# Kernel tuning notes

Measured on AMD Instinct MI355X. Metric: run time of the kernel, lower is better.

## Reference

```python
import jax, jax.numpy as jnp
import numpy as np
from jax.ops import segment_sum

N = 100000   # nodes
E = 6400000  # edges
D = 128      # input/output feature dim (d)
H = 15       # hidden width hard-coded in the module


def setup_inputs() -> dict:
    key = jax.random.key(0)
    ks = jax.random.split(key, 10)
    x = jax.random.normal(ks[0], (N, D), dtype=jnp.float32)
    edge_index = jax.random.randint(ks[1], (2, E), 0, N, dtype=jnp.int64)
    def glorot(k, shape):
        lim = np.sqrt(6.0 / (shape[0] + shape[1]))
        return jax.random.uniform(k, shape, jnp.float32, -lim, lim)
    W1 = glorot(ks[2], (D, H)); b1 = jnp.zeros((H,), jnp.float32)
    W2 = glorot(ks[3], (H, H)); b2 = jnp.zeros((H,), jnp.float32)
    W3 = glorot(ks[4], (H, H)); b3 = jnp.zeros((H,), jnp.float32)
    Wc = glorot(ks[5], (H, D)); bc = jnp.zeros((D,), jnp.float32)
    return {"x": x, "edge_index": edge_index,
            "W1": W1, "b1": b1, "W2": W2, "b2": b2,
            "W3": W3, "b3": b3, "Wc": Wc, "bc": bc}


def _gcn_norm(edge_index, n_nodes):
    # PyG GCNConv default: add self-loops, symmetric normalization.
    loops = jnp.arange(n_nodes, dtype=edge_index.dtype)
    row = jnp.concatenate([edge_index[0], loops])  # source
    col = jnp.concatenate([edge_index[1], loops])  # target (aggregation index)
    deg = segment_sum(jnp.ones_like(col, dtype=jnp.float32), col, num_segments=n_nodes)
    dinv = jnp.where(deg > 0, jax.lax.rsqrt(deg), 0.0)
    norm = dinv[row] * dinv[col]  # [E+N]
    return row, col, norm


def _gcn_conv(x, W, b, row, col, norm, n_nodes):
    h = x @ W                                   # [N, out]
    msg = h[row] * norm[:, None]                # gather + scale
    agg = segment_sum(msg, col, num_segments=n_nodes)
    return agg + b


def reference(x, edge_index, W1, b1, W2, b2, W3, b3, Wc, bc):
    row, col, norm = _gcn_norm(edge_index, N)
    h = jax.nn.relu(_gcn_conv(x, W1, b1, row, col, norm, N))
    h = jax.nn.relu(_gcn_conv(h, W2, b2, row, col, norm, N))
    h = jax.nn.relu(_gcn_conv(h, W3, b3, row, col, norm, N))
    return h @ Wc + bc
```

## Files before the change

### kernel.cpp

```cpp
#include <hip/hip_runtime.h>
#include <hip/hip_fp16.h>

#define DD 128
#define HH 15
#define BSHIFT 8
#define BUCK (1 << BSHIFT)
#define NBUCK 391
#define CAP 18432
#define CHUNK 4096
#define ABLK 512


__global__ __launch_bounds__(512) void init_gcur(int* __restrict__ gcur) {
    int i = threadIdx.x;
    if (i < NBUCK) gcur[i] = i * CAP;
}


__global__ __launch_bounds__(512) void partA(const int* __restrict__ row, const int* __restrict__ col,
                      int* __restrict__ gcur, unsigned* __restrict__ tmp, int E) {
    __shared__ int histo[NBUCK];
    __shared__ int hbase[NBUCK];
    __shared__ int hscan[NBUCK];
    __shared__ int wsum[8];
    __shared__ int s_total;
    __shared__ unsigned staged[CHUNK];
    __shared__ int saddr[CHUNK];
    int tid = threadIdx.x;
    int start = blockIdx.x * CHUNK;
    for (int i = tid; i < NBUCK; i += ABLK) histo[i] = 0;
    __syncthreads();
    unsigned pk[8]; unsigned short lp[8]; unsigned short bk[8];
    for (int k = 0; k < 8; ++k) {
        int e = start + k * ABLK + tid;
        bk[k] = 0xFFFF;
        if (e < E) {
            int cc = col[e];
            int b = cc >> BSHIFT;
            int rr = row[e];
            pk[k] = (unsigned)rr | ((unsigned)(cc & (BUCK - 1)) << 17);
            bk[k] = (unsigned short)b;
            lp[k] = (unsigned short)atomicAdd(&histo[b], 1);
        }
    }
    __syncthreads();
    int lane = tid & 63, wv = tid >> 6;
    int v = (tid < NBUCK) ? histo[tid] : 0;
    int s = v;
#pragma unroll
    for (int off = 1; off < 64; off <<= 1) {
        int u = __shfl_up(s, off, 64);
        if (lane >= off) s += u;
    }
    if (lane == 63) wsum[wv] = s;
    __syncthreads();
    if (tid == 0) {
        int r = 0;
        for (int i = 0; i < 8; ++i) { int u = wsum[i]; wsum[i] = r; r += u; }
        s_total = r;
    }
    __syncthreads();
    if (tid < NBUCK) {
        int excl = s + wsum[wv] - v;
        hscan[tid] = excl;
        if (v > 0) hbase[tid] = atomicAdd(&gcur[tid], v);
    }
    __syncthreads();
    for (int k = 0; k < 8; ++k) {
        if (bk[k] != 0xFFFF) {
            int b = bk[k];
            int slot = hscan[b] + lp[k];
            saddr[slot]  = min(hbase[b] + lp[k], NBUCK * CAP - 1);
            staged[slot] = pk[k];
        }
    }
    __syncthreads();
    int tot = s_total;
    for (int k = tid; k < tot; k += ABLK)
        tmp[saddr[k]] = staged[k];
}


__global__ __launch_bounds__(512) void scanC(const int* __restrict__ gcur,
                                             int* __restrict__ cbase,
                                             int* __restrict__ rowptr, int N) {
    __shared__ int wsum[8];
    int t = threadIdx.x, lane = t & 63, wv = t >> 6;
    int v = 0;
    if (t < NBUCK) v = min(gcur[t] - t * CAP, CAP);
    int s = v;
#pragma unroll
    for (int off = 1; off < 64; off <<= 1) {
        int u = __shfl_up(s, off, 64);
        if (lane >= off) s += u;
    }
    if (lane == 63) wsum[wv] = s;
    __syncthreads();
    int total = 0;
    if (t == 0) { int r = 0; for (int i = 0; i < 8; ++i) { int u = wsum[i]; wsum[i] = r; r += u; } total = r; }
    __syncthreads();
    if (t < NBUCK) cbase[t] = s + wsum[wv] - v;
    if (t == 0) { cbase[NBUCK] = total; rowptr[N] = total; }
}


__global__ __launch_bounds__(1024) void partB(const int* __restrict__ cbase, const unsigned* __restrict__ tmp,
                      int* __restrict__ rowptr, float* __restrict__ dinv,
                      int* __restrict__ csr_row, int N) {
    __shared__ int hist[BUCK];
    __shared__ int cur[BUCK];
    __shared__ int wsum[4];
    int b = blockIdx.x;
    int node0 = b << BSHIFT;
    int nn = min(BUCK, N - node0);
    int tid = threadIdx.x;
    if (tid < BUCK) hist[tid] = 0;
    __syncthreads();
    int base = cbase[b];
    int cnt  = cbase[b + 1] - base;
    const unsigned* te = tmp + (size_t)b * CAP;
    for (int e = tid; e < cnt; e += 1024)
        atomicAdd(&hist[te[e] >> 17], 1);
    __syncthreads();
    int lane = tid & 63, wv = tid >> 6;
    int d0 = (tid < BUCK) ? hist[tid] : 0;
    int s = d0;
#pragma unroll
    for (int off = 1; off < 64; off <<= 1) {
        int u = __shfl_up(s, off, 64);
        if (lane >= off) s += u;
    }
    if (tid < BUCK && lane == 63) wsum[wv] = s;
    __syncthreads();
    if (tid == 0) { int r = 0; for (int i = 0; i < 4; ++i) { int u = wsum[i]; wsum[i] = r; r += u; } }
    __syncthreads();
    if (tid < BUCK) {
        int excl = s + wsum[wv] - d0;
        cur[tid] = base + excl;
        if (tid < nn) {
            rowptr[node0 + tid] = base + excl;
            dinv[node0 + tid] = rsqrtf((float)(d0 + 1));
        }
    }
    __syncthreads();
    for (int e = tid; e < cnt; e += 1024) {
        unsigned v2 = te[e];
        int lc = (int)(v2 >> 17);
        int pos = atomicAdd(&cur[lc], 1);
        csr_row[pos] = (int)(v2 & 0x1FFFFu);
    }
}


__global__ void gemm1_kernel(const float* __restrict__ x, const float* __restrict__ W,
                             const float* __restrict__ dinv, __half* __restrict__ hs) {
    __shared__ float Wl[DD * HH];
    __shared__ float xs[16 * DD];
    int tid = threadIdx.x;
    for (int i = tid; i < DD * HH; i += 256) Wl[i] = W[i];
    size_t base = (size_t)blockIdx.x * 16 * DD;
    const float4* xv = (const float4*)(x + base);
    float4* xsv = (float4*)xs;
    xsv[tid]       = xv[tid];
    xsv[tid + 256] = xv[tid + 256];
    __syncthreads();
    int g = tid >> 4, f = tid & 15;
    int n = blockIdx.x * 16 + g;
    float val = 0.f;
    if (f < HH) {
        const float* xrow = xs + g * DD;
        float acc = 0.f;
#pragma unroll 8
        for (int k = 0; k < DD; ++k) acc += xrow[k] * Wl[k * HH + f];
        val = acc * dinv[n];
    }
    hs[(size_t)n * 16 + f] = __float2half(val);
}


__device__ inline void accU(float4& a0, float4& a1, const uint4& u) {
    float2 f0 = __half22float2(*(const __half2*)&u.x);
    float2 f1 = __half22float2(*(const __half2*)&u.y);
    float2 f2 = __half22float2(*(const __half2*)&u.z);
    float2 f3 = __half22float2(*(const __half2*)&u.w);
    a0.x += f0.x; a0.y += f0.y; a0.z += f1.x; a0.w += f1.y;
    a1.x += f2.x; a1.y += f2.y; a1.z += f3.x; a1.w += f3.y;
}

__device__ inline float4 shfl_down4(float4 v, int off) {
    v.x = __shfl_down(v.x, off, 64);
    v.y = __shfl_down(v.y, off, 64);
    v.z = __shfl_down(v.z, off, 64);
    v.w = __shfl_down(v.w, off, 64);
    return v;
}

template <int FUSE>
__global__ __launch_bounds__(256, 2)
void aggregate_kernel(const int* __restrict__ rowptr, const int* __restrict__ csr_row,
                      const float* __restrict__ dinv, const __half* __restrict__ hs,
                      const float* __restrict__ bias, const float* __restrict__ W,
                      const float* __restrict__ bc,
                      __half* __restrict__ hsout, float* __restrict__ outF, int N) {
    __shared__ float Wl[FUSE == 2 ? HH * DD : 256];
    __shared__ float bs[16];
    __shared__ float bcs[FUSE == 2 ? DD : 1];
    __shared__ float sout[FUSE == 2 ? 16 * DD : 1];
    int tid = threadIdx.x;
    if (FUSE == 1) {
        int k = tid >> 4, f = tid & 15;
        Wl[tid] = (k < HH && f < HH) ? W[k * HH + f] : 0.f;
        if (tid < 16) bs[tid] = (tid < HH) ? bias[tid] : 0.f;
        __syncthreads();
    } else if (FUSE == 2) {
        for (int i = tid; i < HH * DD; i += 256) Wl[i] = W[i];
        if (tid < 16) bs[tid] = (tid < HH) ? bias[tid] : 0.f;
        if (tid < DD) bcs[tid] = bc[tid];
        __syncthreads();
    }
    int wid = (blockIdx.x * 256 + tid) >> 6;
    int lane = tid & 63;
    int sub = lane & 15;
    int c = wid * 4 + (lane >> 4);
    int q = sub & 1, eg = sub >> 1;
    int s = 0, epe = 0;
    if (c < N) { s = rowptr[c]; epe = rowptr[c + 1]; }
    const uint4* h8 = (const uint4*)hs;
    float4 a0 = make_float4(0.f, 0.f, 0.f, 0.f), a1 = a0;
    int e = s + eg;
    for (; e + 56 < epe; e += 64) {
        int i0 = csr_row[e];      int i1 = csr_row[e + 8];
        int i2 = csr_row[e + 16]; int i3 = csr_row[e + 24];
        int i4 = csr_row[e + 32]; int i5 = csr_row[e + 40];
        int i6 = csr_row[e + 48]; int i7 = csr_row[e + 56];
        uint4 v0 = h8[((size_t)i0 << 1) + q];
        uint4 v1 = h8[((size_t)i1 << 1) + q];
        uint4 v2 = h8[((size_t)i2 << 1) + q];
        uint4 v3 = h8[((size_t)i3 << 1) + q];
        uint4 v4 = h8[((size_t)i4 << 1) + q];
        uint4 v5 = h8[((size_t)i5 << 1) + q];
        uint4 v6 = h8[((size_t)i6 << 1) + q];
        uint4 v7 = h8[((size_t)i7 << 1) + q];
        accU(a0, a1, v0); accU(a0, a1, v1); accU(a0, a1, v2); accU(a0, a1, v3);
        accU(a0, a1, v4); accU(a0, a1, v5); accU(a0, a1, v6); accU(a0, a1, v7);
    }
    for (; e + 8 < epe; e += 16) {
        int i0 = csr_row[e]; int i1 = csr_row[e + 8];
        uint4 v0 = h8[((size_t)i0 << 1) + q];
        uint4 v1 = h8[((size_t)i1 << 1) + q];
        accU(a0, a1, v0); accU(a0, a1, v1);
    }
    if (e < epe) {
        uint4 v0 = h8[((size_t)csr_row[e] << 1) + q];
        accU(a0, a1, v0);
    }
#define RED4(off) { float4 t0_ = shfl_down4(a0, off); float4 t1_ = shfl_down4(a1, off); \
                    a0.x += t0_.x; a0.y += t0_.y; a0.z += t0_.z; a0.w += t0_.w; \
                    a1.x += t1_.x; a1.y += t1_.y; a1.z += t1_.z; a1.w += t1_.w; }
    RED4(8) RED4(4) RED4(2)
#undef RED4
    float d = (c < N) ? dinv[c] : 0.f;
    float4 o0 = make_float4(0.f, 0.f, 0.f, 0.f), o1 = o0;
    if (sub < 2 && c < N) {
        uint4 su = h8[((size_t)c << 1) + q];
        float2 s0 = __half22float2(*(const __half2*)&su.x);
        float2 s1 = __half22float2(*(const __half2*)&su.y);
        float2 s2 = __half22float2(*(const __half2*)&su.z);
        float2 s3 = __half22float2(*(const __half2*)&su.w);
        o0.x = d * (a0.x + s0.x); o0.y = d * (a0.y + s0.y);
        o0.z = d * (a0.z + s1.x); o0.w = d * (a0.w + s1.y);
        o1.x = d * (a1.x + s2.x); o1.y = d * (a1.y + s2.y);
        o1.z = d * (a1.z + s3.x); o1.w = d * (a1.w + s3.y);
        int bb = q * 8;
        o0.x = fmaxf(o0.x + bs[bb + 0], 0.f); o0.y = fmaxf(o0.y + bs[bb + 1], 0.f);
        o0.z = fmaxf(o0.z + bs[bb + 2], 0.f); o0.w = fmaxf(o0.w + bs[bb + 3], 0.f);
        o1.x = fmaxf(o1.x + bs[bb + 4], 0.f); o1.y = fmaxf(o1.y + bs[bb + 5], 0.f);
        o1.z = fmaxf(o1.z + bs[bb + 6], 0.f); o1.w = fmaxf(o1.w + bs[bb + 7], 0.f);
    }
    int base = lane & ~15;
    float va[8], vb[8];
    va[0] = __shfl(o0.x, base, 64); va[1] = __shfl(o0.y, base, 64);
    va[2] = __shfl(o0.z, base, 64); va[3] = __shfl(o0.w, base, 64);
    va[4] = __shfl(o1.x, base, 64); va[5] = __shfl(o1.y, base, 64);
    va[6] = __shfl(o1.z, base, 64); va[7] = __shfl(o1.w, base, 64);
    vb[0] = __shfl(o0.x, base + 1, 64); vb[1] = __shfl(o0.y, base + 1, 64);
    vb[2] = __shfl(o0.z, base + 1, 64); vb[3] = __shfl(o0.w, base + 1, 64);
    vb[4] = __shfl(o1.x, base + 1, 64); vb[5] = __shfl(o1.y, base + 1, 64);
    vb[6] = __shfl(o1.z, base + 1, 64); vb[7] = __shfl(o1.w, base + 1, 64);
    if (FUSE == 1) {
        float acc = 0.f;
#pragma unroll
        for (int k = 0; k < 8; ++k) acc += va[k] * Wl[k * 16 + sub];
#pragma unroll
        for (int k = 0; k < 8; ++k) acc += vb[k] * Wl[(8 + k) * 16 + sub];
        if (c < N) hsout[(size_t)c * 16 + sub] = __float2half(acc * d);
    } else if (FUSE == 2) {
        int nl = (tid >> 4);
#pragma unroll
        for (int j = 0; j < 8; ++j) {
            int f = sub + 16 * j;
            float acc = bcs[f];
#pragma unroll
            for (int k = 0; k < 8; ++k)  acc += va[k] * Wl[k * DD + f];
#pragma unroll
            for (int k = 0; k < 7; ++k)  acc += vb[k] * Wl[(8 + k) * DD + f];
            sout[nl * DD + f] = acc;
        }
        __syncthreads();
        int n0 = blockIdx.x * 16;
        const float4* sv = (const float4*)sout;
#pragma unroll
        for (int r = 0; r < 2; ++r) {
            int idx = tid + 256 * r;
            int node = idx >> 5, rem = idx & 31;
            if (n0 + node < N)
                ((float4*)outF)[((size_t)(n0 + node) * DD >> 2) + rem] = sv[idx];
        }
    }
}


extern "C" void kernel_launch(void* const* d_in, const int* in_sizes, int n_in,
                              void* d_out, int out_size, void* d_ws, size_t ws_size,
                              hipStream_t stream) {
    const float* x  = (const float*)d_in[0];
    const int*   ei = (const int*)d_in[1];
    const float* W1 = (const float*)d_in[2];
    const float* b1 = (const float*)d_in[3];
    const float* W2 = (const float*)d_in[4];
    const float* b2 = (const float*)d_in[5];
    const float* W3 = (const float*)d_in[6];
    const float* b3 = (const float*)d_in[7];
    const float* Wc = (const float*)d_in[8];
    const float* bc = (const float*)d_in[9];
    float* out = (float*)d_out;

    int N = in_sizes[0] / DD;
    int E = in_sizes[1] / 2;
    const int* row = ei;
    const int* col = ei + E;

    char* ws = (char*)d_ws;
    size_t off = 0;
    auto alloc = [&](size_t bytes) {
        void* p = ws + off;
        off += (bytes + 255) & ~(size_t)255;
        return p;
    };
    float*    dinv    = (float*)   alloc((size_t)N * 4);
    int*      rowptr  = (int*)     alloc((size_t)(N + 1) * 4);
    int*      gcur    = (int*)     alloc((size_t)NBUCK * 4);
    int*      cbase   = (int*)     alloc((size_t)(NBUCK + 1) * 4);
    int*      csr_row = (int*)     alloc((size_t)E * 4 + 256);
    unsigned* tmp     = (unsigned*)alloc((size_t)NBUCK * CAP * 4);
    (void)n_in; (void)out_size; (void)ws_size;

    __half* hsA = (__half*)tmp;
    __half* hsB = (__half*)((char*)tmp + (size_t)N * 32);

    int eblocks = (E + CHUNK - 1) / CHUNK;

    init_gcur<<<1, 512, 0, stream>>>(gcur);
    partA<<<eblocks, ABLK, 0, stream>>>(row, col, gcur, tmp, E);
    scanC<<<1, 512, 0, stream>>>(gcur, cbase, rowptr, N);
    partB<<<NBUCK, 1024, 0, stream>>>(cbase, tmp, rowptr, dinv, csr_row, N);

    int nb16 = (N + 15) / 16;
    int aggblocks = (N + 15) / 16;

    gemm1_kernel<<<nb16, 256, 0, stream>>>(x, W1, dinv, hsA);
    aggregate_kernel<1><<<aggblocks, 256, 0, stream>>>(rowptr, csr_row, dinv, hsA,
                                                       b1, W2, nullptr, hsB, nullptr, N);
    aggregate_kernel<1><<<aggblocks, 256, 0, stream>>>(rowptr, csr_row, dinv, hsB,
                                                       b2, W3, nullptr, hsA, nullptr, N);
    aggregate_kernel<2><<<aggblocks, 256, 0, stream>>>(rowptr, csr_row, dinv, hsA,
                                                       b3, Wc, bc, nullptr, out, N);
}
```

Measured before the change: 395.8 us.

## Drop global scan with bucket-local CSR, fuse first GEMM into partB, prefetch indices

The global scanC kernel is removed. Each bucket keeps its fixed CAP-strided region in csr_row, and the rows are addressed through separate rowstart/rowend arrays instead of a compact rowptr. When the workspace has room, the first-layer x@W1 projection scaled by dinv is fused into partB, which removes a launch and lets h live in dedicated buffers. The aggregation loop also software-prefetches the next batch of 8 neighbour indices. In exchange the workspace grows, partB uses more shared memory and does more work per block, and the aggregation kernel uses more registers.

```diff
diff --git a/kernel.cpp b/kernel.cpp
--- a/kernel.cpp
+++ b/kernel.cpp
@@ -9,6 +9,7 @@
 #define CAP 18432
 #define CHUNK 4096
 #define ABLK 512
+#define XSTR 132
 
 
 __global__ __launch_bounds__(512) void init_gcur(int* __restrict__ gcur) {
@@ -81,44 +82,28 @@
 }
 
 
-__global__ __launch_bounds__(512) void scanC(const int* __restrict__ gcur,
-                                             int* __restrict__ cbase,
-                                             int* __restrict__ rowptr, int N) {
-    __shared__ int wsum[8];
-    int t = threadIdx.x, lane = t & 63, wv = t >> 6;
-    int v = 0;
-    if (t < NBUCK) v = min(gcur[t] - t * CAP, CAP);
-    int s = v;
-#pragma unroll
-    for (int off = 1; off < 64; off <<= 1) {
-        int u = __shfl_up(s, off, 64);
-        if (lane >= off) s += u;
-    }
-    if (lane == 63) wsum[wv] = s;
-    __syncthreads();
-    int total = 0;
-    if (t == 0) { int r = 0; for (int i = 0; i < 8; ++i) { int u = wsum[i]; wsum[i] = r; r += u; } total = r; }
-    __syncthreads();
-    if (t < NBUCK) cbase[t] = s + wsum[wv] - v;
-    if (t == 0) { cbase[NBUCK] = total; rowptr[N] = total; }
-}
-
-
-__global__ __launch_bounds__(1024) void partB(const int* __restrict__ cbase, const unsigned* __restrict__ tmp,
-                      int* __restrict__ rowptr, float* __restrict__ dinv,
-                      int* __restrict__ csr_row, int N) {
+template <int FG>
+__global__ __launch_bounds__(1024) void partB(const int* __restrict__ gcur, const unsigned* __restrict__ tmp,
+                      int* __restrict__ rowstart, int* __restrict__ rowend,
+                      float* __restrict__ dinv, int* __restrict__ csr_row,
+                      const float* __restrict__ x, const float* __restrict__ W1,
+                      __half* __restrict__ hs, int N) {
     __shared__ int hist[BUCK];
     __shared__ int cur[BUCK];
     __shared__ int wsum[4];
+    __shared__ float sdv[BUCK];
+    __shared__ float Wl[FG ? DD * HH : 1];
+    __shared__ float xs[FG ? 64 * XSTR : 1];
     int b = blockIdx.x;
     int node0 = b << BSHIFT;
     int nn = min(BUCK, N - node0);
     int tid = threadIdx.x;
     if (tid < BUCK) hist[tid] = 0;
-    __syncthreads();
-    int base = cbase[b];
-    int cnt  = cbase[b + 1] - base;
-    const unsigned* te = tmp + (size_t)b * CAP;
+    if (FG) for (int i = tid; i < DD * HH; i += 1024) Wl[i] = W1[i];
+    __syncthreads();
+    int base = b * CAP;
+    int cnt  = min(gcur[b] - base, CAP);
+    const unsigned* te = tmp + (size_t)base;
     for (int e = tid; e < cnt; e += 1024)
         atomicAdd(&hist[te[e] >> 17], 1);
     __syncthreads();
@@ -138,8 +123,11 @@
         int excl = s + wsum[wv] - d0;
         cur[tid] = base + excl;
         if (tid < nn) {
-            rowptr[node0 + tid] = base + excl;
-            dinv[node0 + tid] = rsqrtf((float)(d0 + 1));
+            rowstart[node0 + tid] = base + excl;
+            rowend[node0 + tid]   = base + excl + d0;
+            float dv = rsqrtf((float)(d0 + 1));
+            dinv[node0 + tid] = dv;
+            sdv[tid] = dv;
         }
     }
     __syncthreads();
@@ -149,18 +137,41 @@
         int pos = atomicAdd(&cur[lc], 1);
         csr_row[pos] = (int)(v2 & 0x1FFFFu);
     }
+    if (FG) {
+        for (int p = 0; p < 4; ++p) {
+            __syncthreads();
+            for (int j = tid; j < 64 * 32; j += 1024) {
+                int r = j >> 5, cidx = j & 31;
+                int n = node0 + p * 64 + r;
+                float4 vx = make_float4(0.f, 0.f, 0.f, 0.f);
+                if (n < N) vx = ((const float4*)x)[(size_t)n * 32 + cidx];
+                ((float4*)(xs + r * XSTR))[cidx] = vx;
+            }
+            __syncthreads();
+            int r = tid >> 4, f = tid & 15;
+            int n = node0 + p * 64 + r;
+            float acc = 0.f;
+            if (f < HH) {
+                const float* xr = xs + r * XSTR;
+#pragma unroll 8
+                for (int k = 0; k < DD; ++k) acc += xr[k] * Wl[k * HH + f];
+                acc *= sdv[p * 64 + r];
+            }
+            if (n < N) hs[(size_t)n * 16 + f] = __float2half(acc);
+        }
+    }
 }
 
 
 __global__ void gemm1_kernel(const float* __restrict__ x, const float* __restrict__ W,
                              const float* __restrict__ dinv, __half* __restrict__ hs) {
     __shared__ float Wl[DD * HH];
-    __shared__ float xs[16 * DD];
+    __shared__ float xsl[16 * DD];
     int tid = threadIdx.x;
     for (int i = tid; i < DD * HH; i += 256) Wl[i] = W[i];
     size_t base = (size_t)blockIdx.x * 16 * DD;
     const float4* xv = (const float4*)(x + base);
-    float4* xsv = (float4*)xs;
+    float4* xsv = (float4*)xsl;
     xsv[tid]       = xv[tid];
     xsv[tid + 256] = xv[tid + 256];
     __syncthreads();
@@ -168,7 +179,7 @@
     int n = blockIdx.x * 16 + g;
     float val = 0.f;
     if (f < HH) {
-        const float* xrow = xs + g * DD;
+        const float* xrow = xsl + g * DD;
         float acc = 0.f;
 #pragma unroll 8
         for (int k = 0; k < DD; ++k) acc += xrow[k] * Wl[k * HH + f];
@@ -197,7 +208,8 @@
 
 template <int FUSE>
 __global__ __launch_bounds__(256, 2)
-void aggregate_kernel(const int* __restrict__ rowptr, const int* __restrict__ csr_row,
+void aggregate_kernel(const int* __restrict__ rowstart, const int* __restrict__ rowend,
+                      const int* __restrict__ csr_row,
                       const float* __restrict__ dinv, const __half* __restrict__ hs,
                       const float* __restrict__ bias, const float* __restrict__ W,
                       const float* __restrict__ bc,
@@ -224,15 +236,28 @@
     int c = wid * 4 + (lane >> 4);
     int q = sub & 1, eg = sub >> 1;
     int s = 0, epe = 0;
-    if (c < N) { s = rowptr[c]; epe = rowptr[c + 1]; }
+    if (c < N) { s = rowstart[c]; epe = rowend[c]; }
     const uint4* h8 = (const uint4*)hs;
     float4 a0 = make_float4(0.f, 0.f, 0.f, 0.f), a1 = a0;
     int e = s + eg;
-    for (; e + 56 < epe; e += 64) {
-        int i0 = csr_row[e];      int i1 = csr_row[e + 8];
-        int i2 = csr_row[e + 16]; int i3 = csr_row[e + 24];
-        int i4 = csr_row[e + 32]; int i5 = csr_row[e + 40];
-        int i6 = csr_row[e + 48]; int i7 = csr_row[e + 56];
+    int i0 = 0, i1 = 0, i2 = 0, i3 = 0, i4 = 0, i5 = 0, i6 = 0, i7 = 0;
+    bool have = (e + 56 < epe);
+    if (have) {
+        i0 = csr_row[e];      i1 = csr_row[e + 8];
+        i2 = csr_row[e + 16]; i3 = csr_row[e + 24];
+        i4 = csr_row[e + 32]; i5 = csr_row[e + 40];
+        i6 = csr_row[e + 48]; i7 = csr_row[e + 56];
+    }
+    while (have) {
+        int en = e + 64;
+        bool hn = (en + 56 < epe);
+        int j0 = 0, j1 = 0, j2 = 0, j3 = 0, j4 = 0, j5 = 0, j6 = 0, j7 = 0;
+        if (hn) {
+            j0 = csr_row[en];      j1 = csr_row[en + 8];
+            j2 = csr_row[en + 16]; j3 = csr_row[en + 24];
+            j4 = csr_row[en + 32]; j5 = csr_row[en + 40];
+            j6 = csr_row[en + 48]; j7 = csr_row[en + 56];
+        }
         uint4 v0 = h8[((size_t)i0 << 1) + q];
         uint4 v1 = h8[((size_t)i1 << 1) + q];
         uint4 v2 = h8[((size_t)i2 << 1) + q];
@@ -243,11 +268,13 @@
         uint4 v7 = h8[((size_t)i7 << 1) + q];
         accU(a0, a1, v0); accU(a0, a1, v1); accU(a0, a1, v2); accU(a0, a1, v3);
         accU(a0, a1, v4); accU(a0, a1, v5); accU(a0, a1, v6); accU(a0, a1, v7);
+        i0 = j0; i1 = j1; i2 = j2; i3 = j3; i4 = j4; i5 = j5; i6 = j6; i7 = j7;
+        e = en; have = hn;
     }
     for (; e + 8 < epe; e += 16) {
-        int i0 = csr_row[e]; int i1 = csr_row[e + 8];
-        uint4 v0 = h8[((size_t)i0 << 1) + q];
-        uint4 v1 = h8[((size_t)i1 << 1) + q];
+        int k0 = csr_row[e]; int k1 = csr_row[e + 8];
+        uint4 v0 = h8[((size_t)k0 << 1) + q];
+        uint4 v1 = h8[((size_t)k1 << 1) + q];
         accU(a0, a1, v0); accU(a0, a1, v1);
     }
     if (e < epe) {
@@ -347,32 +374,44 @@
         off += (bytes + 255) & ~(size_t)255;
         return p;
     };
-    float*    dinv    = (float*)   alloc((size_t)N * 4);
-    int*      rowptr  = (int*)     alloc((size_t)(N + 1) * 4);
-    int*      gcur    = (int*)     alloc((size_t)NBUCK * 4);
-    int*      cbase   = (int*)     alloc((size_t)(NBUCK + 1) * 4);
-    int*      csr_row = (int*)     alloc((size_t)E * 4 + 256);
-    unsigned* tmp     = (unsigned*)alloc((size_t)NBUCK * CAP * 4);
-    (void)n_in; (void)out_size; (void)ws_size;
-
-    __half* hsA = (__half*)tmp;
-    __half* hsB = (__half*)((char*)tmp + (size_t)N * 32);
+    float*    dinv     = (float*)   alloc((size_t)N * 4);
+    int*      rowstart = (int*)     alloc((size_t)N * 4);
+    int*      rowend   = (int*)     alloc((size_t)N * 4);
+    int*      gcur     = (int*)     alloc((size_t)NBUCK * 4);
+    int*      csr_row  = (int*)     alloc((size_t)NBUCK * CAP * 4 + 256);
+    unsigned* tmp      = (unsigned*)alloc((size_t)NBUCK * CAP * 4);
+    (void)n_in; (void)out_size;
+
+    size_t hsBytes = (size_t)N * 32;
+    bool roomy = ws_size >= off + 2 * hsBytes + 4096;
+    __half *hsA, *hsB;
+    if (roomy) {
+        hsA = (__half*)alloc(hsBytes);
+        hsB = (__half*)alloc(hsBytes);
+    } else {
+        hsA = (__half*)tmp;
+        hsB = (__half*)((char*)tmp + hsBytes);
+    }
 
     int eblocks = (E + CHUNK - 1) / CHUNK;
 
     init_gcur<<<1, 512, 0, stream>>>(gcur);
     partA<<<eblocks, ABLK, 0, stream>>>(row, col, gcur, tmp, E);
-    scanC<<<1, 512, 0, stream>>>(gcur, cbase, rowptr, N);
-    partB<<<NBUCK, 1024, 0, stream>>>(cbase, tmp, rowptr, dinv, csr_row, N);
-
-    int nb16 = (N + 15) / 16;
+    if (roomy) {
+        partB<1><<<NBUCK, 1024, 0, stream>>>(gcur, tmp, rowstart, rowend, dinv,
+                                             csr_row, x, W1, hsA, N);
+    } else {
+        partB<0><<<NBUCK, 1024, 0, stream>>>(gcur, tmp, rowstart, rowend, dinv,
+                                             csr_row, x, W1, hsA, N);
+        gemm1_kernel<<<(N + 15) / 16, 256, 0, stream>>>(x, W1, dinv, hsA);
+    }
+
     int aggblocks = (N + 15) / 16;
 
-    gemm1_kernel<<<nb16, 256, 0, stream>>>(x, W1, dinv, hsA);
-    aggregate_kernel<1><<<aggblocks, 256, 0, stream>>>(rowptr, csr_row, dinv, hsA,
+    aggregate_kernel<1><<<aggblocks, 256, 0, stream>>>(rowstart, rowend, csr_row, dinv, hsA,
                                                        b1, W2, nullptr, hsB, nullptr, N);
-    aggregate_kernel<1><<<aggblocks, 256, 0, stream>>>(rowptr, csr_row, dinv, hsB,
+    aggregate_kernel<1><<<aggblocks, 256, 0, stream>>>(rowstart, rowend, csr_row, dinv, hsB,
                                                        b2, W3, nullptr, hsA, nullptr, N);
-    aggregate_kernel<2><<<aggblocks, 256, 0, stream>>>(rowptr, csr_row, dinv, hsA,
+    aggregate_kernel<2><<<aggblocks, 256, 0, stream>>>(rowstart, rowend, csr_row, dinv, hsA,
                                                        b3, Wc, bc, nullptr, out, N);
 }
```

Measured after the change: 388.5 us. About the same (-1.8%).
